# Kernel tuning notes

Hardware: AMD Instinct MI355X
Metric: run time of the kernel (lower is better)

The kernel has to match this reference:

```python
import jax, jax.numpy as jnp
import numpy as np

EPS = 1e-6

def _ln(x, w, b):
    m = x.mean(-1, keepdims=True)
    v = ((x - m) ** 2).mean(-1, keepdims=True)
    return (x - m) / jnp.sqrt(v + EPS) * w + b

def setup_inputs() -> dict:
    key = jax.random.key(0)
    ks = jax.random.split(key, 16)
    N, P, C, M = 8192, 64, 128, 4096
    MW = M * P  # 262144 gathered tokens
    A, BL = 131072, 65536
    x = jax.random.normal(ks[0], (N, P, C), dtype=jnp.float32)
    index_window = jax.random.permutation(ks[1], N)[:M]
    index_partition = jax.random.permutation(ks[2], MW)
    perm2 = jax.random.permutation(ks[3], MW)
    asy_index = perm2[:A]
    blocked_index = perm2[A:A + BL]
    p = lambda k, sh: 0.02 * jax.random.normal(k, sh, dtype=jnp.float32)
    return {
        "x": x,
        "index_window": index_window,
        "index_partition": index_partition,
        "asy_index": asy_index,
        "blocked_index": blocked_index,
        "M": M,
        "B": N,
        "ln1_w": jnp.ones((C,), jnp.float32), "ln1_b": jnp.zeros((C,), jnp.float32),
        "qkv_w": p(ks[4], (C, 3 * C)), "qkv_b": jnp.zeros((3 * C,), jnp.float32),
        "proj_w": p(ks[5], (C, C)), "proj_b": jnp.zeros((C,), jnp.float32),
        "gamma1": jnp.full((C,), 1e-1, jnp.float32),
        "ln2_w": jnp.ones((C,), jnp.float32), "ln2_b": jnp.zeros((C,), jnp.float32),
        "mlp_w1": p(ks[6], (C, 4 * C)), "mlp_b1": jnp.zeros((4 * C,), jnp.float32),
        "mlp_w2": p(ks[7], (4 * C, C)), "mlp_b2": jnp.zeros((C,), jnp.float32),
        "gamma2": jnp.full((C,), 1e-1, jnp.float32),
    }

def reference(x, index_window, index_partition, asy_index, blocked_index, M, B,
              ln1_w, ln1_b, qkv_w, qkv_b, proj_w, proj_b, gamma1,
              ln2_w, ln2_b, mlp_w1, mlp_b1, mlp_w2, mlp_b2, gamma2):
    N, P, C = x.shape
    H, dh = 4, 32
    scale = dh ** -0.5
    MW = index_partition.shape[0]
    x = _ln(x, ln1_w, ln1_b)                      # first_norm over whole input
    X = x                                          # (N, P, C)
    xw = x[index_window].reshape(-1, C)            # gather windows -> (MW, C)
    XX = xw
    xa = _ln(xw[asy_index], ln1_w, ln1_b)          # second norm on asy tokens
    xw = xw.at[asy_index].set(xa)
    shortcut = xa                                  # (A, C)
    xp = xw[index_partition].reshape(M, -1, C)     # (M, P, C) attention groups
    qkv = (xp @ qkv_w + qkv_b).reshape(M, P, H, 3 * dh).transpose(0, 2, 1, 3)
    q, k, v = jnp.split(qkv, 3, axis=3)            # each (M, H, P, dh)
    attn = jnp.einsum('mhqd,mhkd->mhqk', q, k) * scale
    # scatter scores keyed by key-token into flat map, mask blocked keys, gather back
    am = jnp.zeros((MW, P, H), attn.dtype)
    am = am.at[index_partition].set(jnp.transpose(attn, (0, 3, 2, 1)).reshape(MW, P, H))
    am = am.at[blocked_index].set(-10000.0)
    attn = jnp.transpose(am[index_partition].reshape(M, P, P, H), (0, 3, 2, 1))
    attn = jax.nn.softmax(attn, axis=-1)
    o = jnp.einsum('mhqk,mhkd->mhqd', attn, v).transpose(0, 2, 1, 3).reshape(M, P, C)
    o = o @ proj_w + proj_b
    XX = XX.at[index_partition].set(o.reshape(-1, C))
    y = XX[asy_index]
    # sub_layers: [ls1, droppath(id), ln2, mlp, ls2, droppath(id)]
    y = y * gamma1                                 # i=0
    y = shortcut + y                               # i=1 residual
    shortcut = y
    y2 = _ln(y, ln2_w, ln2_b)                      # i=2
    y2 = jax.nn.gelu(y2 @ mlp_w1 + mlp_b1, approximate=False) @ mlp_w2 + mlp_b2  # i=3
    y2 = y2 * gamma2                               # i=4
    y = shortcut + y2                              # i=5 residual
    XX = XX.at[asy_index].set(y)
    XX = XX.at[blocked_index].set(X[index_window].reshape(-1, C)[blocked_index])
    X = X.at[index_window].set(XX.reshape(M, -1, C))
    return X
```

## Files before the change

kernel.cpp:

```cpp
#include <hip/hip_runtime.h>
#include <hip/hip_bf16.h>
#include <math.h>

#define N_   8192
#define P_   64
#define C_   128
#define M_   4096
#define MW_  (M_ * P_)
#define A_   131072
#define BL_  65536
#define NROWS_ (N_ * P_)

typedef __attribute__((ext_vector_type(8))) __bf16 bf16x8;
typedef __attribute__((ext_vector_type(4))) float f32x4;
typedef __attribute__((ext_vector_type(2))) __bf16 bf16x2;

__device__ __forceinline__ float wave_sum(float v) {
#pragma unroll
  for (int o = 32; o > 0; o >>= 1) v += __shfl_xor(v, o, 64);
  return v;
}

__global__ __launch_bounds__(256) void k_set8(unsigned char* p, int n) {
  int i = blockIdx.x * 256 + threadIdx.x;
  if (i < n) p[i] = 0;
}
__global__ __launch_bounds__(256) void k_scatter8(unsigned char* p, const int* __restrict__ idx,
                                                  unsigned char v, int n) {
  int i = blockIdx.x * 256 + threadIdx.x;
  if (i < n) p[idx[i]] = v;
}

__global__ __launch_bounds__(256) void k_prep(const float* __restrict__ qkvw,
                                              const float* __restrict__ projw,
                                              __bf16* __restrict__ qkvt,
                                              __bf16* __restrict__ projt) {
  int i = blockIdx.x * 256 + threadIdx.x;
  if (i < 384 * 128) {
    int col = i >> 7, row = i & 127;
    qkvt[i] = (__bf16)qkvw[row * 384 + col];
  } else {
    int j = i - 384 * 128;
    int col = j >> 7, row = j & 127;
    projt[j] = (__bf16)projw[row * 128 + col];
  }
}

__global__ __launch_bounds__(256) void k_prep2(const float* __restrict__ w1,
                                               const float* __restrict__ w2,
                                               __bf16* __restrict__ w1t,
                                               __bf16* __restrict__ w2t) {
  int i = blockIdx.x * 256 + threadIdx.x;
  if (i < 512 * 128) {
    int col = i >> 7, row = i & 127;
    w1t[i] = (__bf16)w1[row * 512 + col];
  } else {
    int j = i - 512 * 128;
    int col = j >> 9, row = j & 511;
    w2t[j] = (__bf16)w2[row * 128 + col];
  }
}

__global__ __launch_bounds__(256) void k_ln_all(const float* __restrict__ x,
                                                const float* __restrict__ w,
                                                const float* __restrict__ b,
                                                float* __restrict__ out) {
  int row = blockIdx.x * 4 + (threadIdx.x >> 6);
  int lane = threadIdx.x & 63;
  float2 xv = ((const float2*)(x + (size_t)row * 128))[lane];
  float mean = wave_sum(xv.x + xv.y) * (1.0f / 128.0f);
  float d0 = xv.x - mean, d1 = xv.y - mean;
  float inv = rsqrtf(wave_sum(d0 * d0 + d1 * d1) * (1.0f / 128.0f) + 1e-6f);
  float2 wv = ((const float2*)w)[lane];
  float2 bv = ((const float2*)b)[lane];
  float2 o2;
  o2.x = d0 * inv * wv.x + bv.x;
  o2.y = d1 * inv * wv.y + bv.y;
  ((float2*)(out + (size_t)row * 128))[lane] = o2;
}

__global__ __launch_bounds__(256, 3) void k_attn(
    const float* __restrict__ x, const int* __restrict__ iw,
    const int* __restrict__ ip, const unsigned char* __restrict__ flags,
    const float* __restrict__ ln1w, const float* __restrict__ ln1b,
    const __bf16* __restrict__ qkvt, const float* __restrict__ qkvb,
    const __bf16* __restrict__ projt, const float* __restrict__ projb,
    float* __restrict__ out) {
  __shared__ __align__(16) __bf16 XV[64 * 132];
  __shared__ __align__(16) __bf16 scratch[4 * 4608];
  __shared__ int srow[64];
  __shared__ unsigned char fl[64];

  const int tid = threadIdx.x;
  const int w = tid >> 6, lane = tid & 63;
  const int quad = lane >> 4, cl = lane & 15;
  const int m = blockIdx.x;

  if (tid < 64) {
    int s = ip[(m << 6) + tid];
    fl[tid] = flags[s];
    srow[tid] = iw[s >> 6] * 64 + (s & 63);
  }
  __syncthreads();

  __bf16* Xs = XV;
  const float lw0 = ln1w[2 * lane], lw1 = ln1w[2 * lane + 1];
  const float lb0 = ln1b[2 * lane], lb1 = ln1b[2 * lane + 1];

  for (int half = 0; half < 2; ++half) {
    float2 xv[8];
#pragma unroll
    for (int ii = 0; ii < 8; ++ii) {
      int r = w + 4 * (half * 8 + ii);
      xv[ii] = ((const float2*)(x + (size_t)srow[r] * 128))[lane];
    }
#pragma unroll
    for (int ii = 0; ii < 8; ++ii) {
      int r = w + 4 * (half * 8 + ii);
      float mean = wave_sum(xv[ii].x + xv[ii].y) * (1.0f / 128.0f);
      float d0 = xv[ii].x - mean, d1 = xv[ii].y - mean;
      float inv = rsqrtf(wave_sum(d0 * d0 + d1 * d1) * (1.0f / 128.0f) + 1e-6f);
      float y0 = d0 * inv * lw0 + lb0, y1 = d1 * inv * lw1 + lb1;
      if (fl[r] == 1) {
        mean = wave_sum(y0 + y1) * (1.0f / 128.0f);
        d0 = y0 - mean; d1 = y1 - mean;
        inv = rsqrtf(wave_sum(d0 * d0 + d1 * d1) * (1.0f / 128.0f) + 1e-6f);
        y0 = d0 * inv * lw0 + lb0; y1 = d1 * inv * lw1 + lb1;
      }
      bf16x2 p2;
      p2[0] = (__bf16)y0; p2[1] = (__bf16)y1;
      *(bf16x2*)&Xs[r * 132 + 2 * lane] = p2;
    }
  }
  __syncthreads();

  __bf16* wsc = scratch + w * 4608;
  __bf16* Qs  = wsc;
  __bf16* Ks  = wsc + 2304;
  __bf16* Vts = XV + w * 2112;
  __bf16* Ps  = wsc;
  __bf16* Os  = wsc;
  const int h = w;

  bf16x8 af[4][4];
#pragma unroll
  for (int mt = 0; mt < 4; ++mt)
#pragma unroll
    for (int kt = 0; kt < 4; ++kt)
      af[mt][kt] = *(const bf16x8*)&Xs[(mt * 16 + cl) * 132 + kt * 32 + quad * 8];
  __syncthreads();

  for (int t = 0; t < 3; ++t) {
#pragma unroll
    for (int nt = 0; nt < 2; ++nt) {
      int col = h * 96 + t * 32 + nt * 16 + cl;
      bf16x8 bfr[4];
#pragma unroll
      for (int kt = 0; kt < 4; ++kt)
        bfr[kt] = *(const bf16x8*)&qkvt[(size_t)col * 128 + kt * 32 + quad * 8];
      float bias = qkvb[col];
#pragma unroll
      for (int mt = 0; mt < 4; ++mt) {
        f32x4 acc = {bias, bias, bias, bias};
#pragma unroll
        for (int kt = 0; kt < 4; ++kt)
          acc = __builtin_amdgcn_mfma_f32_16x16x32_bf16(af[mt][kt], bfr[kt], acc, 0, 0, 0);
        if (t == 0) {
#pragma unroll
          for (int r = 0; r < 4; ++r)
            Qs[(mt * 16 + quad * 4 + r) * 36 + nt * 16 + cl] = (__bf16)acc[r];
        } else if (t == 1) {
#pragma unroll
          for (int r = 0; r < 4; ++r)
            Ks[(mt * 16 + quad * 4 + r) * 36 + nt * 16 + cl] = (__bf16)acc[r];
        } else {
#pragma unroll
          for (int r = 0; r < 4; ++r)
            Vts[(nt * 16 + cl) * 66 + mt * 16 + quad * 4 + r] = (__bf16)acc[r];
        }
      }
    }
  }

  f32x4 sc4[4][4];
  {
    bf16x8 bk[4];
#pragma unroll
    for (int nt = 0; nt < 4; ++nt)
      bk[nt] = *(const bf16x8*)&Ks[(nt * 16 + cl) * 36 + quad * 8];
#pragma unroll
    for (int mt = 0; mt < 4; ++mt) {
      bf16x8 aq = *(const bf16x8*)&Qs[(mt * 16 + cl) * 36 + quad * 8];
#pragma unroll
      for (int nt = 0; nt < 4; ++nt) {
        f32x4 z = {0.f, 0.f, 0.f, 0.f};
        sc4[mt][nt] = __builtin_amdgcn_mfma_f32_16x16x32_bf16(aq, bk[nt], z, 0, 0, 0);
      }
    }
  }
  const float scale = 0.17677669529663687f;
  bool blk[4];
#pragma unroll
  for (int nt = 0; nt < 4; ++nt) blk[nt] = (fl[nt * 16 + cl] == 2);
#pragma unroll
  for (int mt = 0; mt < 4; ++mt)
#pragma unroll
    for (int nt = 0; nt < 4; ++nt)
#pragma unroll
      for (int r = 0; r < 4; ++r) {
        float v = sc4[mt][nt][r];
        sc4[mt][nt][r] = blk[nt] ? -10000.0f : v * scale;
      }
#pragma unroll
  for (int mt = 0; mt < 4; ++mt) {
#pragma unroll
    for (int r = 0; r < 4; ++r) {
      float mx = fmaxf(fmaxf(sc4[mt][0][r], sc4[mt][1][r]),
                       fmaxf(sc4[mt][2][r], sc4[mt][3][r]));
#pragma unroll
      for (int off = 1; off < 16; off <<= 1) mx = fmaxf(mx, __shfl_xor(mx, off, 64));
      float e0 = __expf(sc4[mt][0][r] - mx);
      float e1 = __expf(sc4[mt][1][r] - mx);
      float e2 = __expf(sc4[mt][2][r] - mx);
      float e3 = __expf(sc4[mt][3][r] - mx);
      float sm = (e0 + e1) + (e2 + e3);
#pragma unroll
      for (int off = 1; off < 16; off <<= 1) sm += __shfl_xor(sm, off, 64);
      float inv = 1.0f / sm;
      int row = mt * 16 + quad * 4 + r;
      Ps[row * 68 +  0 + cl] = (__bf16)(e0 * inv);
      Ps[row * 68 + 16 + cl] = (__bf16)(e1 * inv);
      Ps[row * 68 + 32 + cl] = (__bf16)(e2 * inv);
      Ps[row * 68 + 48 + cl] = (__bf16)(e3 * inv);
    }
  }

  f32x4 oacc[4][2];
  {
    bf16x8 bv[2][2];
#pragma unroll
    for (int nt = 0; nt < 2; ++nt)
#pragma unroll
      for (int kt = 0; kt < 2; ++kt)
        bv[nt][kt] = *(const bf16x8*)&Vts[(nt * 16 + cl) * 66 + kt * 32 + quad * 8];
#pragma unroll
    for (int mt = 0; mt < 4; ++mt) {
      bf16x8 ap0 = *(const bf16x8*)&Ps[(mt * 16 + cl) * 68 + quad * 8];
      bf16x8 ap1 = *(const bf16x8*)&Ps[(mt * 16 + cl) * 68 + 32 + quad * 8];
#pragma unroll
      for (int nt = 0; nt < 2; ++nt) {
        f32x4 z = {0.f, 0.f, 0.f, 0.f};
        z = __builtin_amdgcn_mfma_f32_16x16x32_bf16(ap0, bv[nt][0], z, 0, 0, 0);
        z = __builtin_amdgcn_mfma_f32_16x16x32_bf16(ap1, bv[nt][1], z, 0, 0, 0);
        oacc[mt][nt] = z;
      }
    }
  }
#pragma unroll
  for (int mt = 0; mt < 4; ++mt)
#pragma unroll
    for (int nt = 0; nt < 2; ++nt)
#pragma unroll
      for (int r = 0; r < 4; ++r)
        Os[(mt * 16 + quad * 4 + r) * 36 + nt * 16 + cl] = (__bf16)oacc[mt][nt][r];
  __syncthreads();

  const int jw = w * 32;
#pragma unroll
  for (int mt = 0; mt < 4; ++mt) {
#pragma unroll
    for (int nt = 0; nt < 2; ++nt) {
      int col = jw + nt * 16 + cl;
      float pb = projb[col];
      f32x4 acc = {pb, pb, pb, pb};
#pragma unroll
      for (int kt = 0; kt < 4; ++kt) {
        const __bf16* op = scratch + kt * 4608;
        bf16x8 a = *(const bf16x8*)&op[(mt * 16 + cl) * 36 + quad * 8];
        bf16x8 bb = *(const bf16x8*)&projt[(size_t)col * 128 + kt * 32 + quad * 8];
        acc = __builtin_amdgcn_mfma_f32_16x16x32_bf16(a, bb, acc, 0, 0, 0);
      }
#pragma unroll
      for (int r = 0; r < 4; ++r) {
        int row = mt * 16 + quad * 4 + r;
        if (fl[row] != 2)
          out[(size_t)srow[row] * 128 + col] = acc[r];
      }
    }
  }
}

__global__ __launch_bounds__(256) void k_mlp(
    const float* __restrict__ x, const int* __restrict__ iw,
    const int* __restrict__ ia,
    const float* __restrict__ ln1w, const float* __restrict__ ln1b,
    const float* __restrict__ g1,
    const float* __restrict__ ln2w, const float* __restrict__ ln2b,
    const __bf16* __restrict__ w1t, const float* __restrict__ b1,
    const __bf16* __restrict__ w2t, const float* __restrict__ b2,
    const float* __restrict__ g2,
    float* __restrict__ out) {
  __shared__ __align__(16) float ys[64][132];
  __shared__ __align__(16) __bf16 buf[64 * 136];
  __shared__ int wrs[64];

  const int tid = threadIdx.x;
  const int w = tid >> 6, lane = tid & 63;
  const int quad = lane >> 4, cl = lane & 15;

  if (tid < 64) {
    int s = ia[(blockIdx.x << 6) + tid];
    wrs[tid] = iw[s >> 6] * 64 + (s & 63);
  }
  __syncthreads();

  const float lw0 = ln1w[2 * lane], lw1 = ln1w[2 * lane + 1];
  const float lb0 = ln1b[2 * lane], lb1 = ln1b[2 * lane + 1];
  const float g1a = g1[2 * lane], g1b = g1[2 * lane + 1];
  const float l2w0 = ln2w[2 * lane], l2w1 = ln2w[2 * lane + 1];
  const float l2b0 = ln2b[2 * lane], l2b1 = ln2b[2 * lane + 1];

  for (int half = 0; half < 2; ++half) {
    float2 xv[8], ov[8];
#pragma unroll
    for (int ii = 0; ii < 8; ++ii) {
      int r = w + 4 * (half * 8 + ii);
      size_t wr = (size_t)wrs[r];
      xv[ii] = ((const float2*)(x + wr * 128))[lane];
      ov[ii] = ((const float2*)(out + wr * 128))[lane];
    }
#pragma unroll
    for (int ii = 0; ii < 8; ++ii) {
      int r = w + 4 * (half * 8 + ii);
      float mean = wave_sum(xv[ii].x + xv[ii].y) * (1.0f / 128.0f);
      float d0 = xv[ii].x - mean, d1 = xv[ii].y - mean;
      float inv = rsqrtf(wave_sum(d0 * d0 + d1 * d1) * (1.0f / 128.0f) + 1e-6f);
      float y0 = d0 * inv * lw0 + lb0, y1 = d1 * inv * lw1 + lb1;
      mean = wave_sum(y0 + y1) * (1.0f / 128.0f);
      d0 = y0 - mean; d1 = y1 - mean;
      inv = rsqrtf(wave_sum(d0 * d0 + d1 * d1) * (1.0f / 128.0f) + 1e-6f);
      float xa0 = d0 * inv * lw0 + lb0, xa1 = d1 * inv * lw1 + lb1;
      float yv0 = xa0 + g1a * ov[ii].x;
      float yv1 = xa1 + g1b * ov[ii].y;
      ys[r][2 * lane] = yv0;
      ys[r][2 * lane + 1] = yv1;
      mean = wave_sum(yv0 + yv1) * (1.0f / 128.0f);
      d0 = yv0 - mean; d1 = yv1 - mean;
      inv = rsqrtf(wave_sum(d0 * d0 + d1 * d1) * (1.0f / 128.0f) + 1e-6f);
      bf16x2 p2;
      p2[0] = (__bf16)(d0 * inv * l2w0 + l2b0);
      p2[1] = (__bf16)(d1 * inv * l2w1 + l2b1);
      *(bf16x2*)&buf[r * 136 + 2 * lane] = p2;
    }
  }
  __syncthreads();

  bf16x8 af[4][4];
#pragma unroll
  for (int mt = 0; mt < 4; ++mt)
#pragma unroll
    for (int kt = 0; kt < 4; ++kt)
      af[mt][kt] = *(const bf16x8*)&buf[(mt * 16 + cl) * 136 + kt * 32 + quad * 8];
  __syncthreads();

  f32x4 zacc[4][2];
#pragma unroll
  for (int nt = 0; nt < 2; ++nt) {
    float bb = b2[w * 32 + nt * 16 + cl];
#pragma unroll
    for (int mt = 0; mt < 4; ++mt) zacc[mt][nt] = (f32x4){bb, bb, bb, bb};
  }

  for (int ch = 0; ch < 4; ++ch) {
#pragma unroll
    for (int nt = 0; nt < 2; ++nt) {
      int col = ch * 128 + w * 32 + nt * 16 + cl;
      bf16x8 bfr[4];
#pragma unroll
      for (int kt = 0; kt < 4; ++kt)
        bfr[kt] = *(const bf16x8*)&w1t[(size_t)col * 128 + kt * 32 + quad * 8];
      float bias = b1[col];
#pragma unroll
      for (int mt = 0; mt < 4; ++mt) {
        f32x4 acc = {bias, bias, bias, bias};
#pragma unroll
        for (int kt = 0; kt < 4; ++kt)
          acc = __builtin_amdgcn_mfma_f32_16x16x32_bf16(af[mt][kt], bfr[kt], acc, 0, 0, 0);
#pragma unroll
        for (int r = 0; r < 4; ++r) {
          float a = acc[r];
          float g = a * 0.5f * (1.0f + erff(a * 0.70710678118654752f));
          buf[(mt * 16 + quad * 4 + r) * 136 + w * 32 + nt * 16 + cl] = (__bf16)g;
        }
      }
    }
    __syncthreads();
    bf16x8 ah[4][4];
#pragma unroll
    for (int mt = 0; mt < 4; ++mt)
#pragma unroll
      for (int kk = 0; kk < 4; ++kk)
        ah[mt][kk] = *(const bf16x8*)&buf[(mt * 16 + cl) * 136 + kk * 32 + quad * 8];
#pragma unroll
    for (int nt = 0; nt < 2; ++nt) {
      int col = w * 32 + nt * 16 + cl;
      bf16x8 bfr[4];
#pragma unroll
      for (int kk = 0; kk < 4; ++kk)
        bfr[kk] = *(const bf16x8*)&w2t[(size_t)col * 512 + ch * 128 + kk * 32 + quad * 8];
#pragma unroll
      for (int mt = 0; mt < 4; ++mt)
#pragma unroll
        for (int kk = 0; kk < 4; ++kk)
          zacc[mt][nt] = __builtin_amdgcn_mfma_f32_16x16x32_bf16(ah[mt][kk], bfr[kk],
                                                                 zacc[mt][nt], 0, 0, 0);
    }
    __syncthreads();
  }

#pragma unroll
  for (int mt = 0; mt < 4; ++mt)
#pragma unroll
    for (int nt = 0; nt < 2; ++nt) {
      int col = w * 32 + nt * 16 + cl;
      float gg = g2[col];
#pragma unroll
      for (int r = 0; r < 4; ++r) {
        int row = mt * 16 + quad * 4 + r;
        out[(size_t)wrs[row] * 128 + col] = ys[row][col] + gg * zacc[mt][nt][r];
      }
    }
}

extern "C" void kernel_launch(void* const* d_in, const int* in_sizes, int n_in,
                              void* d_out, int out_size, void* d_ws, size_t ws_size,
                              hipStream_t stream) {
  const float* x = (const float*)d_in[0];
  const int* iw = (const int*)d_in[1];
  const int* ip = (const int*)d_in[2];
  const int* ia = (const int*)d_in[3];
  const int* ib = (const int*)d_in[4];
  const float* ln1w = (const float*)d_in[7];
  const float* ln1b = (const float*)d_in[8];
  const float* qkvw = (const float*)d_in[9];
  const float* qkvb = (const float*)d_in[10];
  const float* projw = (const float*)d_in[11];
  const float* projb = (const float*)d_in[12];
  const float* g1 = (const float*)d_in[13];
  const float* ln2w = (const float*)d_in[14];
  const float* ln2b = (const float*)d_in[15];
  const float* w1 = (const float*)d_in[16];
  const float* b1 = (const float*)d_in[17];
  const float* w2 = (const float*)d_in[18];
  const float* b2 = (const float*)d_in[19];
  const float* g2 = (const float*)d_in[20];
  float* out = (float*)d_out;

  unsigned char* flags = (unsigned char*)d_ws;
  __bf16* qkvt = (__bf16*)((char*)d_ws + MW_);
  __bf16* projt = (__bf16*)((char*)d_ws + MW_ + 384 * 128 * 2);
  __bf16* w1t = (__bf16*)((char*)d_ws + MW_ + 384 * 128 * 2 + 128 * 128 * 2);
  __bf16* w2t = (__bf16*)((char*)d_ws + MW_ + 384 * 128 * 2 + 128 * 128 * 2 + 512 * 128 * 2);

  k_set8<<<MW_ / 256, 256, 0, stream>>>(flags, MW_);
  k_scatter8<<<A_ / 256, 256, 0, stream>>>(flags, ia, 1, A_);
  k_scatter8<<<BL_ / 256, 256, 0, stream>>>(flags, ib, 2, BL_);
  k_prep<<<(384 * 128 + 128 * 128) / 256, 256, 0, stream>>>(qkvw, projw, qkvt, projt);
  k_prep2<<<(512 * 128 + 128 * 512) / 256, 256, 0, stream>>>(w1, w2, w1t, w2t);
  k_ln_all<<<NROWS_ / 4, 256, 0, stream>>>(x, ln1w, ln1b, out);
  k_attn<<<M_, 256, 0, stream>>>(x, iw, ip, flags, ln1w, ln1b, qkvt, qkvb,
                                 projt, projb, out);
  k_mlp<<<A_ / 64, 256, 0, stream>>>(x, iw, ia, ln1w, ln1b, g1, ln2w, ln2b,
                                     w1t, b1, w2t, b2, g2, out);
}
```

Baseline: 935.1 us.

## Reuse first-norm output in attention, merge setup kernels, retune LDS padding and priority

The attention kernel now reads the already-normalized rows from the output buffer instead of recomputing the first LayerNorm from x. The two flag-scatter launches become one kernel, and the two weight-prep kernels become one. The change also shrinks LDS row padding for Q/K and the MLP buffers, adds s_setprio around the MFMA blocks, unrolls the QKV loop, and adds an occupancy hint to the MLP kernel. The new padding makes some rows sit off 16-byte boundaries for the 128-bit LDS reads, which can cost bank or alignment penalties.

```diff
diff --git a/kernel.cpp b/kernel.cpp
--- a/kernel.cpp
+++ b/kernel.cpp
@@ -25,37 +25,39 @@
   int i = blockIdx.x * 256 + threadIdx.x;
   if (i < n) p[i] = 0;
 }
-__global__ __launch_bounds__(256) void k_scatter8(unsigned char* p, const int* __restrict__ idx,
-                                                  unsigned char v, int n) {
+__global__ __launch_bounds__(256) void k_scatter2(unsigned char* p,
+                                                  const int* __restrict__ ia,
+                                                  const int* __restrict__ ib) {
   int i = blockIdx.x * 256 + threadIdx.x;
-  if (i < n) p[idx[i]] = v;
+  if (i < A_) p[ia[i]] = 1;
+  else {
+    int j = i - A_;
+    if (j < BL_) p[ib[j]] = 2;
+  }
 }
 
 __global__ __launch_bounds__(256) void k_prep(const float* __restrict__ qkvw,
                                               const float* __restrict__ projw,
+                                              const float* __restrict__ w1,
+                                              const float* __restrict__ w2,
                                               __bf16* __restrict__ qkvt,
-                                              __bf16* __restrict__ projt) {
+                                              __bf16* __restrict__ projt,
+                                              __bf16* __restrict__ w1t,
+                                              __bf16* __restrict__ w2t) {
   int i = blockIdx.x * 256 + threadIdx.x;
   if (i < 384 * 128) {
     int col = i >> 7, row = i & 127;
     qkvt[i] = (__bf16)qkvw[row * 384 + col];
-  } else {
+  } else if (i < 384 * 128 + 128 * 128) {
     int j = i - 384 * 128;
     int col = j >> 7, row = j & 127;
     projt[j] = (__bf16)projw[row * 128 + col];
-  }
-}
-
-__global__ __launch_bounds__(256) void k_prep2(const float* __restrict__ w1,
-                                               const float* __restrict__ w2,
-                                               __bf16* __restrict__ w1t,
-                                               __bf16* __restrict__ w2t) {
-  int i = blockIdx.x * 256 + threadIdx.x;
-  if (i < 512 * 128) {
-    int col = i >> 7, row = i & 127;
-    w1t[i] = (__bf16)w1[row * 512 + col];
+  } else if (i < 384 * 128 + 128 * 128 + 512 * 128) {
+    int j = i - 384 * 128 - 128 * 128;
+    int col = j >> 7, row = j & 127;
+    w1t[j] = (__bf16)w1[row * 512 + col];
   } else {
-    int j = i - 512 * 128;
+    int j = i - 384 * 128 - 128 * 128 - 512 * 128;
     int col = j >> 9, row = j & 511;
     w2t[j] = (__bf16)w2[row * 128 + col];
   }
@@ -80,14 +82,14 @@
 }
 
 __global__ __launch_bounds__(256, 3) void k_attn(
-    const float* __restrict__ x, const int* __restrict__ iw,
+    const int* __restrict__ iw,
     const int* __restrict__ ip, const unsigned char* __restrict__ flags,
     const float* __restrict__ ln1w, const float* __restrict__ ln1b,
     const __bf16* __restrict__ qkvt, const float* __restrict__ qkvb,
     const __bf16* __restrict__ projt, const float* __restrict__ projb,
-    float* __restrict__ out) {
+    float* out) {
   __shared__ __align__(16) __bf16 XV[64 * 132];
-  __shared__ __align__(16) __bf16 scratch[4 * 4608];
+  __shared__ __align__(16) __bf16 scratch[4 * 4352];
   __shared__ int srow[64];
   __shared__ unsigned char fl[64];
 
@@ -112,20 +114,18 @@
 #pragma unroll
     for (int ii = 0; ii < 8; ++ii) {
       int r = w + 4 * (half * 8 + ii);
-      xv[ii] = ((const float2*)(x + (size_t)srow[r] * 128))[lane];
+      xv[ii] = ((const float2*)(out + (size_t)srow[r] * 128))[lane];
     }
 #pragma unroll
     for (int ii = 0; ii < 8; ++ii) {
       int r = w + 4 * (half * 8 + ii);
-      float mean = wave_sum(xv[ii].x + xv[ii].y) * (1.0f / 128.0f);
-      float d0 = xv[ii].x - mean, d1 = xv[ii].y - mean;
-      float inv = rsqrtf(wave_sum(d0 * d0 + d1 * d1) * (1.0f / 128.0f) + 1e-6f);
-      float y0 = d0 * inv * lw0 + lb0, y1 = d1 * inv * lw1 + lb1;
+      float y0 = xv[ii].x, y1 = xv[ii].y;
       if (fl[r] == 1) {
-        mean = wave_sum(y0 + y1) * (1.0f / 128.0f);
-        d0 = y0 - mean; d1 = y1 - mean;
-        inv = rsqrtf(wave_sum(d0 * d0 + d1 * d1) * (1.0f / 128.0f) + 1e-6f);
-        y0 = d0 * inv * lw0 + lb0; y1 = d1 * inv * lw1 + lb1;
+        float mean = wave_sum(y0 + y1) * (1.0f / 128.0f);
+        float d0 = y0 - mean, d1 = y1 - mean;
+        float inv = rsqrtf(wave_sum(d0 * d0 + d1 * d1) * (1.0f / 128.0f) + 1e-6f);
+        y0 = d0 * inv * lw0 + lb0;
+        y1 = d1 * inv * lw1 + lb1;
       }
       bf16x2 p2;
       p2[0] = (__bf16)y0; p2[1] = (__bf16)y1;
@@ -134,9 +134,9 @@
   }
   __syncthreads();
 
-  __bf16* wsc = scratch + w * 4608;
+  __bf16* wsc = scratch + w * 4352;
   __bf16* Qs  = wsc;
-  __bf16* Ks  = wsc + 2304;
+  __bf16* Ks  = wsc + 2176;
   __bf16* Vts = XV + w * 2112;
   __bf16* Ps  = wsc;
   __bf16* Os  = wsc;
@@ -150,6 +150,7 @@
       af[mt][kt] = *(const bf16x8*)&Xs[(mt * 16 + cl) * 132 + kt * 32 + quad * 8];
   __syncthreads();
 
+#pragma unroll
   for (int t = 0; t < 3; ++t) {
 #pragma unroll
     for (int nt = 0; nt < 2; ++nt) {
@@ -159,6 +160,7 @@
       for (int kt = 0; kt < 4; ++kt)
         bfr[kt] = *(const bf16x8*)&qkvt[(size_t)col * 128 + kt * 32 + quad * 8];
       float bias = qkvb[col];
+      __builtin_amdgcn_s_setprio(1);
 #pragma unroll
       for (int mt = 0; mt < 4; ++mt) {
         f32x4 acc = {bias, bias, bias, bias};
@@ -168,17 +170,18 @@
         if (t == 0) {
 #pragma unroll
           for (int r = 0; r < 4; ++r)
-            Qs[(mt * 16 + quad * 4 + r) * 36 + nt * 16 + cl] = (__bf16)acc[r];
+            Qs[(mt * 16 + quad * 4 + r) * 34 + nt * 16 + cl] = (__bf16)acc[r];
         } else if (t == 1) {
 #pragma unroll
           for (int r = 0; r < 4; ++r)
-            Ks[(mt * 16 + quad * 4 + r) * 36 + nt * 16 + cl] = (__bf16)acc[r];
+            Ks[(mt * 16 + quad * 4 + r) * 34 + nt * 16 + cl] = (__bf16)acc[r];
         } else {
 #pragma unroll
           for (int r = 0; r < 4; ++r)
             Vts[(nt * 16 + cl) * 66 + mt * 16 + quad * 4 + r] = (__bf16)acc[r];
         }
       }
+      __builtin_amdgcn_s_setprio(0);
     }
   }
 
@@ -187,16 +190,18 @@
     bf16x8 bk[4];
 #pragma unroll
     for (int nt = 0; nt < 4; ++nt)
-      bk[nt] = *(const bf16x8*)&Ks[(nt * 16 + cl) * 36 + quad * 8];
+      bk[nt] = *(const bf16x8*)&Ks[(nt * 16 + cl) * 34 + quad * 8];
+    __builtin_amdgcn_s_setprio(1);
 #pragma unroll
     for (int mt = 0; mt < 4; ++mt) {
-      bf16x8 aq = *(const bf16x8*)&Qs[(mt * 16 + cl) * 36 + quad * 8];
+      bf16x8 aq = *(const bf16x8*)&Qs[(mt * 16 + cl) * 34 + quad * 8];
 #pragma unroll
       for (int nt = 0; nt < 4; ++nt) {
         f32x4 z = {0.f, 0.f, 0.f, 0.f};
         sc4[mt][nt] = __builtin_amdgcn_mfma_f32_16x16x32_bf16(aq, bk[nt], z, 0, 0, 0);
       }
     }
+    __builtin_amdgcn_s_setprio(0);
   }
   const float scale = 0.17677669529663687f;
   bool blk[4];
@@ -243,6 +248,7 @@
 #pragma unroll
       for (int kt = 0; kt < 2; ++kt)
         bv[nt][kt] = *(const bf16x8*)&Vts[(nt * 16 + cl) * 66 + kt * 32 + quad * 8];
+    __builtin_amdgcn_s_setprio(1);
 #pragma unroll
     for (int mt = 0; mt < 4; ++mt) {
       bf16x8 ap0 = *(const bf16x8*)&Ps[(mt * 16 + cl) * 68 + quad * 8];
@@ -255,6 +261,7 @@
         oacc[mt][nt] = z;
       }
     }
+    __builtin_amdgcn_s_setprio(0);
   }
 #pragma unroll
   for (int mt = 0; mt < 4; ++mt)
@@ -275,7 +282,7 @@
       f32x4 acc = {pb, pb, pb, pb};
 #pragma unroll
       for (int kt = 0; kt < 4; ++kt) {
-        const __bf16* op = scratch + kt * 4608;
+        const __bf16* op = scratch + kt * 4352;
         bf16x8 a = *(const bf16x8*)&op[(mt * 16 + cl) * 36 + quad * 8];
         bf16x8 bb = *(const bf16x8*)&projt[(size_t)col * 128 + kt * 32 + quad * 8];
         acc = __builtin_amdgcn_mfma_f32_16x16x32_bf16(a, bb, acc, 0, 0, 0);
@@ -290,7 +297,7 @@
   }
 }
 
-__global__ __launch_bounds__(256) void k_mlp(
+__global__ __launch_bounds__(256, 3) void k_mlp(
     const float* __restrict__ x, const int* __restrict__ iw,
     const int* __restrict__ ia,
     const float* __restrict__ ln1w, const float* __restrict__ ln1b,
@@ -300,8 +307,8 @@
     const __bf16* __restrict__ w2t, const float* __restrict__ b2,
     const float* __restrict__ g2,
     float* __restrict__ out) {
-  __shared__ __align__(16) float ys[64][132];
-  __shared__ __align__(16) __bf16 buf[64 * 136];
+  __shared__ __align__(16) float ys[64][130];
+  __shared__ __align__(16) __bf16 buf[64 * 132];
   __shared__ int wrs[64];
 
   const int tid = threadIdx.x;
@@ -350,7 +357,7 @@
       bf16x2 p2;
       p2[0] = (__bf16)(d0 * inv * l2w0 + l2b0);
       p2[1] = (__bf16)(d1 * inv * l2w1 + l2b1);
-      *(bf16x2*)&buf[r * 136 + 2 * lane] = p2;
+      *(bf16x2*)&buf[r * 132 + 2 * lane] = p2;
     }
   }
   __syncthreads();
@@ -360,7 +367,7 @@
   for (int mt = 0; mt < 4; ++mt)
 #pragma unroll
     for (int kt = 0; kt < 4; ++kt)
-      af[mt][kt] = *(const bf16x8*)&buf[(mt * 16 + cl) * 136 + kt * 32 + quad * 8];
+      af[mt][kt] = *(const bf16x8*)&buf[(mt * 16 + cl) * 132 + kt * 32 + quad * 8];
   __syncthreads();
 
   f32x4 zacc[4][2];
@@ -380,6 +387,7 @@
       for (int kt = 0; kt < 4; ++kt)
         bfr[kt] = *(const bf16x8*)&w1t[(size_t)col * 128 + kt * 32 + quad * 8];
       float bias = b1[col];
+      __builtin_amdgcn_s_setprio(1);
 #pragma unroll
       for (int mt = 0; mt < 4; ++mt) {
         f32x4 acc = {bias, bias, bias, bias};
@@ -390,9 +398,10 @@
         for (int r = 0; r < 4; ++r) {
           float a = acc[r];
           float g = a * 0.5f * (1.0f + erff(a * 0.70710678118654752f));
-          buf[(mt * 16 + quad * 4 + r) * 136 + w * 32 + nt * 16 + cl] = (__bf16)g;
+          buf[(mt * 16 + quad * 4 + r) * 132 + w * 32 + nt * 16 + cl] = (__bf16)g;
         }
       }
+      __builtin_amdgcn_s_setprio(0);
     }
     __syncthreads();
     bf16x8 ah[4][4];
@@ -400,7 +409,7 @@
     for (int mt = 0; mt < 4; ++mt)
 #pragma unroll
       for (int kk = 0; kk < 4; ++kk)
-        ah[mt][kk] = *(const bf16x8*)&buf[(mt * 16 + cl) * 136 + kk * 32 + quad * 8];
+        ah[mt][kk] = *(const bf16x8*)&buf[(mt * 16 + cl) * 132 + kk * 32 + quad * 8];
 #pragma unroll
     for (int nt = 0; nt < 2; ++nt) {
       int col = w * 32 + nt * 16 + cl;
@@ -408,12 +417,14 @@
 #pragma unroll
       for (int kk = 0; kk < 4; ++kk)
         bfr[kk] = *(const bf16x8*)&w2t[(size_t)col * 512 + ch * 128 + kk * 32 + quad * 8];
+      __builtin_amdgcn_s_setprio(1);
 #pragma unroll
       for (int mt = 0; mt < 4; ++mt)
 #pragma unroll
         for (int kk = 0; kk < 4; ++kk)
           zacc[mt][nt] = __builtin_amdgcn_mfma_f32_16x16x32_bf16(ah[mt][kk], bfr[kk],
                                                                  zacc[mt][nt], 0, 0, 0);
+      __builtin_amdgcn_s_setprio(0);
     }
     __syncthreads();
   }
@@ -463,12 +474,11 @@
   __bf16* w2t = (__bf16*)((char*)d_ws + MW_ + 384 * 128 * 2 + 128 * 128 * 2 + 512 * 128 * 2);
 
   k_set8<<<MW_ / 256, 256, 0, stream>>>(flags, MW_);
-  k_scatter8<<<A_ / 256, 256, 0, stream>>>(flags, ia, 1, A_);
-  k_scatter8<<<BL_ / 256, 256, 0, stream>>>(flags, ib, 2, BL_);
-  k_prep<<<(384 * 128 + 128 * 128) / 256, 256, 0, stream>>>(qkvw, projw, qkvt, projt);
-  k_prep2<<<(512 * 128 + 128 * 512) / 256, 256, 0, stream>>>(w1, w2, w1t, w2t);
+  k_scatter2<<<(A_ + BL_) / 256, 256, 0, stream>>>(flags, ia, ib);
+  k_prep<<<(384 * 128 + 128 * 128 + 512 * 128 + 128 * 512) / 256, 256, 0, stream>>>(
+      qkvw, projw, w1, w2, qkvt, projt, w1t, w2t);
   k_ln_all<<<NROWS_ / 4, 256, 0, stream>>>(x, ln1w, ln1b, out);
-  k_attn<<<M_, 256, 0, stream>>>(x, iw, ip, flags, ln1w, ln1b, qkvt, qkvb,
+  k_attn<<<M_, 256, 0, stream>>>(iw, ip, flags, ln1w, ln1b, qkvt, qkvb,
                                  projt, projb, out);
   k_mlp<<<A_ / 64, 256, 0, stream>>>(x, iw, ia, ln1w, ln1b, g1, ln2w, ln2b,
                                      w1t, b1, w2t, b2, g2, out);
```

After: 881.3 us. 5.8% less time.
